# Performance work log

Measured on AMD Instinct MI355X. Metric: run time of the kernel, lower is better.

Reference implementation:

```python
import jax, jax.numpy as jnp
import numpy as np

# Quantum circuit math: each wire starts in |0>, gets RX(x_i) (encoder), then a
# single-qubit, the n-wire state is a product state and each wire's <Z> is
# analytically cos(theta_i) * cos(x_i):
#   RX(x)|0> = [cos(x/2), -i sin(x/2)];  after RY(th):
#   <Z> = (cos^2(th/2)-sin^2(th/2)) * (cos^2(x/2)-sin^2(x/2)) = cos(th)cos(x).
# This is exactly the math the torchquantum simulator computes, expressed in
# closed form (no 2^d_k state vector needed).

NUM_HEADS = 64


def setup_inputs() -> dict:
    key = jax.random.key(0)
    k1, k2, k3 = jax.random.split(key, 3)
    B, T, E = 4, 1024, 512
    d_k = E // NUM_HEADS  # 8 wires
    x = jax.random.normal(k1, (B, T, E), dtype=jnp.float32)
    theta = jax.random.normal(k2, (d_k,), dtype=jnp.float32)  # shared RY params (one QLayer reused across heads)
    W_combine = jax.random.normal(k3, (E, E), dtype=jnp.float32) * (E ** -0.5)
    b_combine = jnp.zeros((E,), dtype=jnp.float32)
    return {"x": x, "theta": theta, "W_combine": W_combine, "b_combine": b_combine}


def reference(x, theta, W_combine, b_combine):
    B, T, E = x.shape
    H = NUM_HEADS
    d_k = E // H
    # split heads: [B, H, T, d_k]
    xh = x.reshape(B, T, H, d_k).transpose(0, 2, 1, 3)
    # quantum layer output: per-wire PauliZ expectation = cos(theta) * cos(x)
    proj = jnp.cos(xh) * jnp.cos(theta)  # [B, H, T, d_k]
    # self-attention on quantum projections
    scale = 1.0 / (d_k ** 0.5)
    scores = jnp.einsum('bhtd,bhsd->bhts', proj, proj) * scale  # [B, H, T, T]
    probs = jax.nn.softmax(scores, axis=-1)
    # dropout is identity in eval mode
    attn = jnp.einsum('bhts,bhsd->bhtd', probs, proj)  # [B, H, T, d_k]
    out = attn.transpose(0, 2, 1, 3).reshape(B, T, E)
    return out @ W_combine.T + b_combine
```

## Files before the change

### kernel.cpp

```cpp
#include <hip/hip_runtime.h>
#include <hip/hip_bf16.h>
#include <cstdint>
#include <cstddef>

#define T_DIM 1024
#define E_DIM 512

typedef short bf16x8 __attribute__((ext_vector_type(8)));
typedef float f32x4  __attribute__((ext_vector_type(4)));
typedef float f32x16 __attribute__((ext_vector_type(16)));

__global__ __launch_bounds__(512, 4)
void qattn_mfma(const float* __restrict__ x,
                const float* __restrict__ theta,
                const float* __restrict__ W,
                __hip_bfloat16* __restrict__ attn_out,
                __hip_bfloat16* __restrict__ w_bf)
{
    __shared__ __align__(16) char shraw[16384 + 20640];
    auto projA = (__hip_bfloat16 (*)[8])(shraw);
    auto projT = (__hip_bfloat16 (*)[1032])(shraw + 16384);

    const int p    = blockIdx.x;
    const int xcd  = p & 7;
    const int idx  = p >> 3;
    const int head = xcd * 32 + (idx >> 1);
    const int qh   = idx & 1;
    const int b    = head >> 6;
    const int h    = head & 63;
    const int tid  = threadIdx.x;
    const int lane = tid & 63;
    const int wv   = tid >> 6;
    const int l31  = lane & 31;
    const int hf   = lane >> 5;

    {
        const int gid = p * 512 + tid;
        if (gid < 65536) {
            const float4 v = *(const float4*)(W + gid * 4);
            alignas(8) __hip_bfloat16 ob[4] = {
                __float2bfloat16(v.x), __float2bfloat16(v.y),
                __float2bfloat16(v.z), __float2bfloat16(v.w)};
            *(uint2*)(w_bf + gid * 4) = *(const uint2*)ob;
        }
    }

    const float SA2 = 8.0804315f;
    float ctT[8], ctA[8];
#pragma unroll
    for (int d = 0; d < 8; ++d) {
        ctT[d] = __cosf(theta[d]);
        ctA[d] = ctT[d] * SA2;
    }

    const float* xb = x + (size_t)b * T_DIM * E_DIM + h * 8;
#pragma unroll
    for (int rr = 0; rr < 2; ++rr) {
        const int r = tid + rr * 512;
        const float4 v0 = *(const float4*)(xb + (size_t)r * E_DIM);
        const float4 v1 = *(const float4*)(xb + (size_t)r * E_DIM + 4);
        float pr[8] = {v0.x, v0.y, v0.z, v0.w, v1.x, v1.y, v1.z, v1.w};
        alignas(16) __hip_bfloat16 ra[8];
#pragma unroll
        for (int d = 0; d < 8; ++d) {
            const float c = __cosf(pr[d]);
            ra[d] = __float2bfloat16(c * ctA[d]);
            projT[d][r] = __float2bfloat16(c * ctT[d]);
        }
        *(uint4*)&projA[r][0] = *(const uint4*)ra;
        projT[8][r] = __ushort_as_bfloat16((unsigned short)0x3f80);
        projT[9][r] = __ushort_as_bfloat16((unsigned short)0);
    }
    __syncthreads();

    const bf16x8 z8 = {};

    const float MAGIC = 8404858.0f;
    f32x16 cinit;
#pragma unroll
    for (int i = 0; i < 16; ++i) cinit[i] = MAGIC;

    const int q0 = qh * 512 + wv * 64;
    bf16x8 bq[2];
#pragma unroll
    for (int qt = 0; qt < 2; ++qt)
        bq[qt] = (hf == 0) ? *(const bf16x8*)&projA[q0 + qt * 32 + l31][0]
                           : z8;

    f32x16 nacc[2] = {};

    const __hip_bfloat16* kabase =
        (hf == 0) ? &projA[l31][0] : &projA[0][0];
    const int bvrow = (l31 < 8) ? l31 : ((l31 == 8) ? 8 : 9);
    const __hip_bfloat16* bvbase = &projT[bvrow][hf * 4];

#pragma unroll
    for (int kc = 0; kc < 32; ++kc) {
        const int key0 = kc * 32;
        const bf16x8 ka = *(const bf16x8*)(kabase + (size_t)key0 * 8);

        union { uint2 u[2]; bf16x8 v; } bA, bB;
        bA.u[0] = *(const uint2*)(bvbase + key0);
        bA.u[1] = *(const uint2*)(bvbase + key0 + 8);
        bB.u[0] = *(const uint2*)(bvbase + key0 + 16);
        bB.u[1] = *(const uint2*)(bvbase + key0 + 24);

#pragma unroll
        for (int qt = 0; qt < 2; ++qt) {
            const f32x16 s = __builtin_amdgcn_mfma_f32_32x32x16_bf16(
                ka, bq[qt], cinit, 0, 0, 0);

            union { f32x16 f; uint32_t u[16]; } a;
            a.f = s;
            union { uint32_t u[4]; bf16x8 v; } pA, pB;
#pragma unroll
            for (int i = 0; i < 4; ++i) {
                pA.u[i] = __builtin_amdgcn_perm(a.u[2 * i + 1], a.u[2 * i],
                                                0x05040100u);
                pB.u[i] = __builtin_amdgcn_perm(a.u[8 + 2 * i + 1],
                                                a.u[8 + 2 * i], 0x05040100u);
            }
            nacc[qt] = __builtin_amdgcn_mfma_f32_32x32x16_bf16(
                pA.v, bA.v, nacc[qt], 0, 0, 0);
            nacc[qt] = __builtin_amdgcn_mfma_f32_32x32x16_bf16(
                pB.v, bB.v, nacc[qt], 0, 0, 0);
        }
    }

    const int denSrc = (lane & 32) | 8;
#pragma unroll
    for (int qt = 0; qt < 2; ++qt) {
#pragma unroll
        for (int r = 0; r < 16; ++r) {
            const float den = __shfl(nacc[qt][r], denSrc);
            const float inv = __builtin_amdgcn_rcpf(den);
            if (l31 < 8) {
                const int qrow = q0 + qt * 32 + (r & 3) + 8 * (r >> 2) + 4 * hf;
                attn_out[(size_t)(b * T_DIM + qrow) * E_DIM + h * 8 + l31] =
                    __float2bfloat16(nacc[qt][r] * inv);
            }
        }
    }
}

#define BM 64
#define BN 64
#define BK 64

__global__ __launch_bounds__(256, 2)
void combine_gemm(const __hip_bfloat16* __restrict__ A,
                  const __hip_bfloat16* __restrict__ Wb,
                  const float* __restrict__ bias,
                  float* __restrict__ out)
{
    __shared__ __hip_bfloat16 As[BM][BK];
    __shared__ __hip_bfloat16 Bs[BN][BK];

    const int tid  = threadIdx.x;
    const int lane = tid & 63;
    const int wave = tid >> 6;
    const int bm   = blockIdx.x;
    const int bn   = blockIdx.y;
    const int wm   = (wave & 1) * 32;
    const int wn   = (wave >> 1) * 32;
    const int rlo  = lane & 15;
    const int quad = lane >> 4;

    f32x4 acc[2][2] = {};

    for (int k0 = 0; k0 < E_DIM; k0 += BK) {
        if (k0) __syncthreads();
#pragma unroll
        for (int pp = 0; pp < 2; ++pp) {
            const int c   = pp * 256 + tid;
            const int row = c >> 3;
            const int kcs = c & 7;
            const int kc  = kcs ^ (row & 7);
            const __hip_bfloat16* gA =
                A + (size_t)(bm * BM + row) * E_DIM + k0 + kc * 8;
            char* lA = (char*)As + (size_t)(pp * 256 + wave * 64) * 16;
            __builtin_amdgcn_global_load_lds(
                (const __attribute__((address_space(1))) void*)gA,
                (__attribute__((address_space(3))) void*)lA, 16, 0, 0);
        }
#pragma unroll
        for (int pp = 0; pp < 2; ++pp) {
            const int c   = pp * 256 + tid;
            const int row = c >> 3;
            const int kcs = c & 7;
            const int kc  = kcs ^ (row & 7);
            const __hip_bfloat16* gW =
                Wb + (size_t)(bn * BN + row) * E_DIM + k0 + kc * 8;
            char* lB = (char*)Bs + (size_t)(pp * 256 + wave * 64) * 16;
            __builtin_amdgcn_global_load_lds(
                (const __attribute__((address_space(1))) void*)gW,
                (__attribute__((address_space(3))) void*)lB, 16, 0, 0);
        }
        __syncthreads();

#pragma unroll
        for (int ks = 0; ks < 2; ++ks) {
            const int kci  = ks * 4 + quad;
            const int koff = (kci ^ (rlo & 7)) * 8;
            bf16x8 af[2], bf[2];
#pragma unroll
            for (int i = 0; i < 2; ++i)
                af[i] = *(const bf16x8*)&As[wm + i * 16 + rlo][koff];
#pragma unroll
            for (int j = 0; j < 2; ++j)
                bf[j] = *(const bf16x8*)&Bs[wn + j * 16 + rlo][koff];
#pragma unroll
            for (int i = 0; i < 2; ++i)
#pragma unroll
                for (int j = 0; j < 2; ++j)
                    acc[i][j] = __builtin_amdgcn_mfma_f32_16x16x32_bf16(
                        af[i], bf[j], acc[i][j], 0, 0, 0);
        }
    }

    const int row0 = bm * BM + wm;
    const int col0 = bn * BN + wn;
#pragma unroll
    for (int j = 0; j < 2; ++j) {
        const int col = col0 + j * 16 + rlo;
        const float bv = bias[col];
#pragma unroll
        for (int i = 0; i < 2; ++i) {
            const int rbase = row0 + i * 16 + quad * 4;
#pragma unroll
            for (int r = 0; r < 4; ++r)
                out[(size_t)(rbase + r) * E_DIM + col] = acc[i][j][r] + bv;
        }
    }
}

extern "C" void kernel_launch(void* const* d_in, const int* in_sizes, int n_in,
                              void* d_out, int out_size, void* d_ws,
                              size_t ws_size, hipStream_t stream)
{
    const float* x     = (const float*)d_in[0];
    const float* theta = (const float*)d_in[1];
    const float* W     = (const float*)d_in[2];
    const float* bias  = (const float*)d_in[3];
    float* out = (float*)d_out;

    __hip_bfloat16* attn_bf = (__hip_bfloat16*)d_ws;
    __hip_bfloat16* w_bf    = (__hip_bfloat16*)((char*)d_ws + 4u * 1024u * 1024u);

    hipLaunchKernelGGL(qattn_mfma, dim3(512), dim3(512), 0, stream,
                       x, theta, W, attn_bf, w_bf);
    hipLaunchKernelGGL(combine_gemm, dim3(64, 8), dim3(256), 0, stream,
                       attn_bf, w_bf, bias, out);
}
```

Measured before the change: 92.05 us.

## Double-buffer combine GEMM tiles, use K8 score MFMA, and hoist x loads

The combine GEMM now keeps two LDS buffers, so the async global-to-LDS load of the next K tile overlaps the MFMAs on the current one, with one barrier per iteration instead of two. In the attention kernel, the score computation switches to the 32x32x8 bf16 MFMA when the builtin is available. That matches the 8-wide head dimension instead of zero-padding a K=16 instruction. All four x loads are also issued before the cosine and convert work, to expose memory-level parallelism. The risk is that the older K8 instruction may not issue at a faster rate than the K16 one on this hardware, and double buffering doubles the GEMM's LDS footprint.

```diff
diff --git a/kernel.cpp b/kernel.cpp
--- a/kernel.cpp
+++ b/kernel.cpp
@@ -6,9 +6,16 @@
 #define T_DIM 1024
 #define E_DIM 512
 
+typedef short bf16x4 __attribute__((ext_vector_type(4)));
 typedef short bf16x8 __attribute__((ext_vector_type(8)));
 typedef float f32x4  __attribute__((ext_vector_type(4)));
 typedef float f32x16 __attribute__((ext_vector_type(16)));
+
+#if __has_builtin(__builtin_amdgcn_mfma_f32_32x32x8bf16_1k)
+#define SCORE_K8 1
+#else
+#define SCORE_K8 0
+#endif
 
 __global__ __launch_bounds__(512, 4)
 void qattn_mfma(const float* __restrict__ x,
@@ -54,11 +61,15 @@
     }
 
     const float* xb = x + (size_t)b * T_DIM * E_DIM + h * 8;
+    const float4 va0 = *(const float4*)(xb + (size_t)tid * E_DIM);
+    const float4 va1 = *(const float4*)(xb + (size_t)tid * E_DIM + 4);
+    const float4 vb0 = *(const float4*)(xb + (size_t)(tid + 512) * E_DIM);
+    const float4 vb1 = *(const float4*)(xb + (size_t)(tid + 512) * E_DIM + 4);
 #pragma unroll
     for (int rr = 0; rr < 2; ++rr) {
         const int r = tid + rr * 512;
-        const float4 v0 = *(const float4*)(xb + (size_t)r * E_DIM);
-        const float4 v1 = *(const float4*)(xb + (size_t)r * E_DIM + 4);
+        const float4 v0 = rr ? vb0 : va0;
+        const float4 v1 = rr ? vb1 : va1;
         float pr[8] = {v0.x, v0.y, v0.z, v0.w, v1.x, v1.y, v1.z, v1.w};
         alignas(16) __hip_bfloat16 ra[8];
 #pragma unroll
@@ -73,31 +84,43 @@
     }
     __syncthreads();
 
-    const bf16x8 z8 = {};
-
     const float MAGIC = 8404858.0f;
     f32x16 cinit;
 #pragma unroll
     for (int i = 0; i < 16; ++i) cinit[i] = MAGIC;
 
     const int q0 = qh * 512 + wv * 64;
+
+#if SCORE_K8
+    bf16x4 bq4[2];
+#pragma unroll
+    for (int qt = 0; qt < 2; ++qt)
+        bq4[qt] = *(const bf16x4*)&projA[q0 + qt * 32 + l31][hf * 4];
+    const __hip_bfloat16* kabase = &projA[l31][hf * 4];
+#else
+    const bf16x8 z8 = {};
     bf16x8 bq[2];
 #pragma unroll
     for (int qt = 0; qt < 2; ++qt)
         bq[qt] = (hf == 0) ? *(const bf16x8*)&projA[q0 + qt * 32 + l31][0]
                            : z8;
-
-    f32x16 nacc[2] = {};
-
     const __hip_bfloat16* kabase =
         (hf == 0) ? &projA[l31][0] : &projA[0][0];
+#endif
+
+    f32x16 nacc[2] = {};
+
     const int bvrow = (l31 < 8) ? l31 : ((l31 == 8) ? 8 : 9);
     const __hip_bfloat16* bvbase = &projT[bvrow][hf * 4];
 
 #pragma unroll
     for (int kc = 0; kc < 32; ++kc) {
         const int key0 = kc * 32;
+#if SCORE_K8
+        const bf16x4 ka4 = *(const bf16x4*)(kabase + (size_t)key0 * 8);
+#else
         const bf16x8 ka = *(const bf16x8*)(kabase + (size_t)key0 * 8);
+#endif
 
         union { uint2 u[2]; bf16x8 v; } bA, bB;
         bA.u[0] = *(const uint2*)(bvbase + key0);
@@ -107,8 +130,13 @@
 
 #pragma unroll
         for (int qt = 0; qt < 2; ++qt) {
+#if SCORE_K8
+            const f32x16 s = __builtin_amdgcn_mfma_f32_32x32x8bf16_1k(
+                ka4, bq4[qt], cinit, 0, 0, 0);
+#else
             const f32x16 s = __builtin_amdgcn_mfma_f32_32x32x16_bf16(
                 ka, bq[qt], cinit, 0, 0, 0);
+#endif
 
             union { f32x16 f; uint32_t u[16]; } a;
             a.f = s;
@@ -153,8 +181,8 @@
                   const float* __restrict__ bias,
                   float* __restrict__ out)
 {
-    __shared__ __hip_bfloat16 As[BM][BK];
-    __shared__ __hip_bfloat16 Bs[BN][BK];
+    __shared__ __hip_bfloat16 As[2][BM][BK];
+    __shared__ __hip_bfloat16 Bs[2][BN][BK];
 
     const int tid  = threadIdx.x;
     const int lane = tid & 63;
@@ -168,8 +196,7 @@
 
     f32x4 acc[2][2] = {};
 
-    for (int k0 = 0; k0 < E_DIM; k0 += BK) {
-        if (k0) __syncthreads();
+    auto stage = [&](int buf, int k0) {
 #pragma unroll
         for (int pp = 0; pp < 2; ++pp) {
             const int c   = pp * 256 + tid;
@@ -178,7 +205,8 @@
             const int kc  = kcs ^ (row & 7);
             const __hip_bfloat16* gA =
                 A + (size_t)(bm * BM + row) * E_DIM + k0 + kc * 8;
-            char* lA = (char*)As + (size_t)(pp * 256 + wave * 64) * 16;
+            char* lA = (char*)&As[buf][0][0] +
+                       (size_t)(pp * 256 + wave * 64) * 16;
             __builtin_amdgcn_global_load_lds(
                 (const __attribute__((address_space(1))) void*)gA,
                 (__attribute__((address_space(3))) void*)lA, 16, 0, 0);
@@ -191,12 +219,21 @@
             const int kc  = kcs ^ (row & 7);
             const __hip_bfloat16* gW =
                 Wb + (size_t)(bn * BN + row) * E_DIM + k0 + kc * 8;
-            char* lB = (char*)Bs + (size_t)(pp * 256 + wave * 64) * 16;
+            char* lB = (char*)&Bs[buf][0][0] +
+                       (size_t)(pp * 256 + wave * 64) * 16;
             __builtin_amdgcn_global_load_lds(
                 (const __attribute__((address_space(1))) void*)gW,
                 (__attribute__((address_space(3))) void*)lB, 16, 0, 0);
         }
-        __syncthreads();
+    };
+
+    stage(0, 0);
+    __syncthreads();
+
+#pragma unroll
+    for (int t = 0; t < 8; ++t) {
+        const int cb = t & 1;
+        if (t + 1 < 8) stage(cb ^ 1, (t + 1) * BK);
 
 #pragma unroll
         for (int ks = 0; ks < 2; ++ks) {
@@ -205,10 +242,10 @@
             bf16x8 af[2], bf[2];
 #pragma unroll
             for (int i = 0; i < 2; ++i)
-                af[i] = *(const bf16x8*)&As[wm + i * 16 + rlo][koff];
+                af[i] = *(const bf16x8*)&As[cb][wm + i * 16 + rlo][koff];
 #pragma unroll
             for (int j = 0; j < 2; ++j)
-                bf[j] = *(const bf16x8*)&Bs[wn + j * 16 + rlo][koff];
+                bf[j] = *(const bf16x8*)&Bs[cb][wn + j * 16 + rlo][koff];
 #pragma unroll
             for (int i = 0; i < 2; ++i)
 #pragma unroll
@@ -216,6 +253,7 @@
                     acc[i][j] = __builtin_amdgcn_mfma_f32_16x16x32_bf16(
                         af[i], bf[j], acc[i][j], 0, 0, 0);
         }
+        __syncthreads();
     }
 
     const int row0 = bm * BM + wm;
```

Measured after the change: 92.28 us. Within noise of the previous version (+0.3%).
